# Kernel optimization log

Hardware: AMD Instinct MI355X
Metric: run time of the kernel (lower is better)

Reference implementation:

```python
import jax, jax.numpy as jnp
import numpy as np

B, L, ENC_IN, C_OUT = 8, 2048, 21, 21
D_MODEL, EXPAND, D_STATE, D_CONV = 512, 2, 16, 4
D_INNER = D_MODEL * EXPAND
DT_RANK = (D_MODEL + 15) // 16  # 'auto' => ceil(d_model/16) = 32
MARK_DIM = 4  # timeF features for freq='h'
PRED_LEN = 96


def setup_inputs() -> dict:
    key = jax.random.key(0)
    ks = jax.random.split(key, 13)
    s = 0.02
    return {
        'x_enc': jax.random.normal(ks[0], (B, L, ENC_IN), jnp.float32),
        'x_mark_enc': jax.random.normal(ks[1], (B, L, MARK_DIM), jnp.float32),
        'x_dec': jax.random.normal(ks[2], (B, PRED_LEN, ENC_IN), jnp.float32),
        'x_mark_dec': jax.random.normal(ks[3], (B, PRED_LEN, MARK_DIM), jnp.float32),
        'conv_w': jax.random.normal(ks[4], (D_MODEL, ENC_IN, 3), jnp.float32) * s,      # TokenEmbedding circular conv
        'temp_w': jax.random.normal(ks[5], (D_MODEL, MARK_DIM), jnp.float32) * s,       # TimeFeatureEmbedding (no bias)
        'in_proj_w': jax.random.normal(ks[6], (2 * D_INNER, D_MODEL), jnp.float32) * s,
        'conv1d_w': jax.random.normal(ks[7], (D_INNER, 1, D_CONV), jnp.float32) * s,    # depthwise causal conv
        'conv1d_b': jnp.zeros((D_INNER,), jnp.float32),
        'x_proj_w': jax.random.normal(ks[8], (DT_RANK + 2 * D_STATE, D_INNER), jnp.float32) * s,
        'dt_proj_w': jax.random.normal(ks[9], (D_INNER, DT_RANK), jnp.float32) * s,
        'dt_proj_b': jax.random.normal(ks[10], (D_INNER,), jnp.float32) * 0.1,
        'A_log': jnp.log(jnp.tile(jnp.arange(1, D_STATE + 1, dtype=jnp.float32), (D_INNER, 1))),  # mamba S4D-real init
        'D': jnp.ones((D_INNER,), jnp.float32),
        'out_proj_w': jax.random.normal(ks[11], (D_MODEL, D_INNER), jnp.float32) * s,
        'head_w': jax.random.normal(ks[12], (C_OUT, D_MODEL), jnp.float32) * s,
    }


def _pos_embedding(seq_len, d):
    pos = jnp.arange(seq_len, dtype=jnp.float32)[:, None]
    div = jnp.exp(jnp.arange(0, d, 2, dtype=jnp.float32) * (-np.log(10000.0) / d))
    pe = jnp.zeros((seq_len, d), jnp.float32)
    pe = pe.at[:, 0::2].set(jnp.sin(pos * div))
    pe = pe.at[:, 1::2].set(jnp.cos(pos * div))
    return pe


def _mamba(x, in_proj_w, conv1d_w, conv1d_b, x_proj_w, dt_proj_w, dt_proj_b, A_log, D):
    Bsz = x.shape[0]
    xz = x @ in_proj_w.T                          # (B,L,2*Din)
    xs, z = jnp.split(xz, 2, axis=-1)
    # causal depthwise conv1d over time (pad left d_conv-1, truncate to L)
    xc = jnp.pad(xs.transpose(0, 2, 1), ((0, 0), (0, 0), (D_CONV - 1, 0)))
    xc = jax.lax.conv_general_dilated(xc, conv1d_w, (1,), 'VALID',
                                      dimension_numbers=('NCH', 'OIH', 'NCH'),
                                      feature_group_count=D_INNER)
    xs = jax.nn.silu((xc + conv1d_b[None, :, None]).transpose(0, 2, 1))  # (B,L,Din)
    x_dbl = xs @ x_proj_w.T                       # (B,L,dt_rank+2N)
    dt, Bm, Cm = jnp.split(x_dbl, [DT_RANK, DT_RANK + D_STATE], axis=-1)
    delta = jax.nn.softplus(dt @ dt_proj_w.T + dt_proj_b)  # (B,L,Din)
    A = -jnp.exp(A_log)                           # (Din,N)

    def step(h, inp):
        u_t, d_t, b_t, c_t = inp                  # (B,Din),(B,Din),(B,N),(B,N)
        dA = jnp.exp(d_t[:, :, None] * A)         # (B,Din,N)
        h = dA * h + (d_t * u_t)[:, :, None] * b_t[:, None, :]
        return h, jnp.einsum('bdn,bn->bd', h, c_t)

    h0 = jnp.zeros((Bsz, D_INNER, D_STATE), xs.dtype)
    seq = (xs.transpose(1, 0, 2), delta.transpose(1, 0, 2),
           Bm.transpose(1, 0, 2), Cm.transpose(1, 0, 2))
    _, ys = jax.lax.scan(step, h0, seq)
    y = ys.transpose(1, 0, 2) + xs * D            # (B,L,Din)
    return y * jax.nn.silu(z)


def _forward(x_enc, x_mark_enc, conv_w, temp_w, in_proj_w, conv1d_w, conv1d_b,
             x_proj_w, dt_proj_w, dt_proj_b, A_log, D, out_proj_w, head_w):
    # RevIN-style instance norm over time (stats detached)
    mean = jax.lax.stop_gradient(jnp.mean(x_enc, axis=1, keepdims=True))
    xc = x_enc - mean
    std = jax.lax.stop_gradient(jnp.sqrt(jnp.var(xc, axis=1, keepdims=True) + 1e-5))
    xn = xc / std
    # TokenEmbedding: circular-padded conv1d, kernel 3, no bias
    xt = jnp.pad(xn.transpose(0, 2, 1), ((0, 0), (0, 0), (1, 1)), mode='wrap')
    val = jax.lax.conv_general_dilated(xt, conv_w, (1,), 'VALID',
                                       dimension_numbers=('NCH', 'OIH', 'NCH')).transpose(0, 2, 1)
    emb = val + x_mark_enc @ temp_w.T + _pos_embedding(x_enc.shape[1], D_MODEL)[None]
    y = _mamba(emb, in_proj_w, conv1d_w, conv1d_b, x_proj_w, dt_proj_w, dt_proj_b, A_log, D)
    y = y @ out_proj_w.T                          # Mamba out_proj (no bias)
    out = y @ head_w.T                            # final Linear (no bias)
    out = out * std + mean                        # de-normalize
    return out[:, -PRED_LEN:, :]


def reference(x_enc, x_mark_enc, x_dec, x_mark_dec, conv_w, temp_w, in_proj_w,
              conv1d_w, conv1d_b, x_proj_w, dt_proj_w, dt_proj_b, A_log, D,
              out_proj_w, head_w):
    # x_dec / x_mark_dec are accepted but unused by the forecast path
    return _forward(x_enc, x_mark_enc, conv_w, temp_w, in_proj_w, conv1d_w,
                    conv1d_b, x_proj_w, dt_proj_w, dt_proj_b, A_log, D,
                    out_proj_w, head_w)
```

## Files before the change

kernel.cpp:

```cpp
#include <hip/hip_runtime.h>
#include <hip/hip_bf16.h>
#include <math.h>

#define Bsz 8
#define Lseq 2048
#define ENC_IN 21
#define C_OUT 21
#define D_MODEL 512
#define D_INNER 1024
#define D_STATE 16
#define D_CONV 4
#define DT_RANK 32
#define MARK_DIM 4
#define PRED_LEN 96
#define L_TAIL (Lseq - PRED_LEN)
#define K_EMB 80
#define CHUNK 128
#define NCHUNK_A 15
#define MTOT (Bsz * Lseq)

#define PE_C0 (-9.210340371976184f / (float)D_MODEL)

typedef __attribute__((ext_vector_type(8))) short short8;
typedef __attribute__((ext_vector_type(4))) float f32x4;

__global__ void stats_kernel(const float* __restrict__ x_enc,
                             float* __restrict__ mean, float* __restrict__ stdv) {
    int bc = blockIdx.x;
    int b = bc / ENC_IN, c = bc % ENC_IN;
    __shared__ float red[256];
    int t = threadIdx.x;
    float s = 0.f;
    for (int l = t; l < Lseq; l += 256)
        s += x_enc[((size_t)b * Lseq + l) * ENC_IN + c];
    red[t] = s; __syncthreads();
    for (int off = 128; off > 0; off >>= 1) {
        if (t < off) red[t] += red[t + off];
        __syncthreads();
    }
    float m = red[0] / (float)Lseq;
    __syncthreads();
    float v = 0.f;
    for (int l = t; l < Lseq; l += 256) {
        float d = x_enc[((size_t)b * Lseq + l) * ENC_IN + c] - m;
        v += d * d;
    }
    red[t] = v; __syncthreads();
    for (int off = 128; off > 0; off >>= 1) {
        if (t < off) red[t] += red[t + off];
        __syncthreads();
    }
    if (t == 0) {
        mean[bc] = m;
        stdv[bc] = sqrtf(red[0] / (float)Lseq + 1e-5f);
    }
}

__global__ void fuse_w_kernel(const float* __restrict__ head_w,
                              const float* __restrict__ out_proj_w,
                              float* __restrict__ W) {
    int idx = blockIdx.x * 256 + threadIdx.x;
    if (idx >= C_OUT * D_INNER) return;
    int c = idx / D_INNER, d = idx % D_INNER;
    float s = 0.f;
    for (int k = 0; k < D_MODEL; ++k)
        s += head_w[c * D_MODEL + k] * out_proj_w[(size_t)k * D_INNER + d];
    W[idx] = s;
}

__global__ void prep_wT_kernel(const float* __restrict__ conv_w,
                               const float* __restrict__ temp_w,
                               float* __restrict__ WembT) {
    int idx = blockIdx.x * 256 + threadIdx.x;
    int k = idx / D_MODEL, d = idx % D_MODEL;
    float v = 0.f;
    if (k < 3 * ENC_IN) {
        int kk = k / ENC_IN, c = k % ENC_IN;
        v = conv_w[((size_t)d * ENC_IN + c) * 3 + kk];
    } else if (k < 3 * ENC_IN + MARK_DIM) {
        v = temp_w[d * MARK_DIM + (k - 3 * ENC_IN)];
    }
    WembT[idx] = v;
}

__global__ void prep_x_kernel(const float* __restrict__ x_enc,
                              const float* __restrict__ x_mark,
                              const float* __restrict__ mean,
                              const float* __restrict__ stdv,
                              float* __restrict__ xinT) {
    int idx = blockIdx.x * 256 + threadIdx.x;
    int k = idx >> 14, bl = idx & (MTOT - 1);
    int b = bl >> 11, l = bl & (Lseq - 1);
    float v = 0.f;
    if (k < 3 * ENC_IN) {
        int kk = k / ENC_IN, c = k % ENC_IN;
        int ll = (l + kk - 1 + Lseq) & (Lseq - 1);
        v = (x_enc[((size_t)b * Lseq + ll) * ENC_IN + c] - mean[b * ENC_IN + c])
            / stdv[b * ENC_IN + c];
    } else if (k < 3 * ENC_IN + MARK_DIM) {
        v = x_mark[((size_t)b * Lseq + l) * MARK_DIM + (k - 3 * ENC_IN)];
    }
    xinT[idx] = v;
}

__global__ void wcomb_kernel(const float* __restrict__ in_proj_w,
                             const float* __restrict__ WembT,
                             float* __restrict__ Wcomb) {
    int idx = blockIdx.x * 256 + threadIdx.x;
    int j = idx / K_EMB, k = idx % K_EMB;
    const float* a = in_proj_w + (size_t)j * D_MODEL;
    const float* b = WembT + (size_t)k * D_MODEL;
    float s = 0.f;
    for (int d = 0; d < D_MODEL; d += 4) {
        float4 av = *(const float4*)(a + d);
        float4 bv = *(const float4*)(b + d);
        s += av.x * bv.x + av.y * bv.y + av.z * bv.z + av.w * bv.w;
    }
    Wcomb[idx] = s;
}

__global__ void pepz_kernel(const float* __restrict__ in_proj_w,
                            float* __restrict__ PEpZ) {
    __shared__ float per[D_MODEL];
    int lz = blockIdx.x;
    int t = threadIdx.x;
    {
        int l = L_TAIL + lz;
        float div = __expf((float)(2 * t) * PE_C0);
        float s, c;
        sincosf((float)l * div, &s, &c);
        per[2 * t] = s;
        per[2 * t + 1] = c;
    }
    __syncthreads();
    for (int q = 0; q < 4; ++q) {
        int j = q * 256 + t;
        const float* w = in_proj_w + (size_t)(D_INNER + j) * D_MODEL;
        float s = 0.f;
        for (int d = 0; d < D_MODEL; d += 4) {
            float4 wv = *(const float4*)(w + d);
            s += per[d] * wv.x + per[d + 1] * wv.y + per[d + 2] * wv.z + per[d + 3] * wv.w;
        }
        PEpZ[(size_t)lz * D_INNER + j] = s;
    }
}

template <int AMODE, int BMODE, int EPI>
__launch_bounds__(256)
__global__ void gemm(const float* __restrict__ A, const float* __restrict__ B,
                     float* __restrict__ C0, const float* __restrict__ bias,
                     int M, int N, int K, int lda, int ldb) {
    __shared__ float As[16][65];
    __shared__ float Bs[16][65];
    int bm = blockIdx.y, bn = blockIdx.x;
    int t = threadIdx.x;
    int tx = t & 15, ty = t >> 4;
    float acc[4][4] = {};
    int arow = bm * 64, bcol = bn * 64;
    int lr = t >> 2;
    int lk = (t & 3) * 4;
    int lrk = t >> 4;
    int lm4 = (t & 15) * 4;

    size_t acol = 0;
    if constexpr (AMODE == 2) {
        int m0 = arow + lm4;
        acol = (size_t)(m0 / PRED_LEN) * Lseq + L_TAIL + (m0 % PRED_LEN);
    } else if constexpr (AMODE == 1) {
        acol = (size_t)(arow + lm4);
    }

    for (int k0 = 0; k0 < K; k0 += 16) {
        if constexpr (AMODE == 0) {
            float4 av = *(const float4*)(A + (size_t)(arow + lr) * lda + k0 + lk);
            As[lk + 0][lr] = av.x; As[lk + 1][lr] = av.y;
            As[lk + 2][lr] = av.z; As[lk + 3][lr] = av.w;
        } else {
            float4 av = *(const float4*)(A + (size_t)(k0 + lrk) * lda + acol);
            As[lrk][lm4 + 0] = av.x; As[lrk][lm4 + 1] = av.y;
            As[lrk][lm4 + 2] = av.z; As[lrk][lm4 + 3] = av.w;
        }
        if constexpr (BMODE == 0) {
            float4 bv = *(const float4*)(B + (size_t)(bcol + lr) * ldb + k0 + lk);
            Bs[lk + 0][lr] = bv.x; Bs[lk + 1][lr] = bv.y;
            Bs[lk + 2][lr] = bv.z; Bs[lk + 3][lr] = bv.w;
        } else {
            float4 bv = *(const float4*)(B + (size_t)(k0 + lrk) * ldb + bcol + lm4);
            Bs[lrk][lm4 + 0] = bv.x; Bs[lrk][lm4 + 1] = bv.y;
            Bs[lrk][lm4 + 2] = bv.z; Bs[lrk][lm4 + 3] = bv.w;
        }
        __syncthreads();
        #pragma unroll
        for (int kk = 0; kk < 16; ++kk) {
            float a[4], bq[4];
            #pragma unroll
            for (int i = 0; i < 4; ++i) a[i] = As[kk][ty * 4 + i];
            #pragma unroll
            for (int j = 0; j < 4; ++j) bq[j] = Bs[kk][tx * 4 + j];
            #pragma unroll
            for (int i = 0; i < 4; ++i)
                #pragma unroll
                for (int j = 0; j < 4; ++j)
                    acc[i][j] += a[i] * bq[j];
        }
        __syncthreads();
    }

    #pragma unroll
    for (int i = 0; i < 4; ++i) {
        int row = arow + ty * 4 + i;
        #pragma unroll
        for (int j = 0; j < 4; ++j) {
            int col = bcol + tx * 4 + j;
            float v = acc[i][j];
            if (EPI == 3) {
                v += bias[(size_t)(row % PRED_LEN) * N + col];
            }
            C0[(size_t)row * N + col] = v;
        }
    }
}

__device__ __forceinline__ void split_bf16(float x, short& hb, short& lb) {
    unsigned u = __float_as_uint(x);
    unsigned short h = (unsigned short)(u >> 16);
    float hf = __uint_as_float(((unsigned)h) << 16);
    unsigned short l = (unsigned short)(__float_as_uint(x - hf) >> 16);
    hb = (short)h; lb = (short)l;
}

template <int BMODE, int EPI>
__launch_bounds__(256)
__global__ void mfma_gemm(const float* __restrict__ A, const float* __restrict__ B,
                          float* __restrict__ C, const float* __restrict__ bias,
                          int M, int N, int K, int lda, int ldb) {
    __shared__ short Ah[64][48], Al[64][48];
    __shared__ short Bh[64][48], Bl[64][48];
    int t = threadIdx.x;
    int bn0 = blockIdx.x * 64;
    int am0 = blockIdx.y * 64;
    int w = t >> 6;
    int l = t & 63;
    int lr = l & 15;
    int lk = l >> 4;

    f32x4 acc[4];
    #pragma unroll
    for (int i = 0; i < 4; ++i) acc[i] = (f32x4){0.f, 0.f, 0.f, 0.f};

    const int mst = t >> 2, kst = (t & 3) * 8;

    for (int kb = 0; kb < K; kb += 32) {
        if (kb) __syncthreads();
        {
            const float* src = A + (size_t)(am0 + mst) * lda + kb + kst;
            short8 hv, lv;
            if (kb + 32 <= K) {
                float4 a0 = *(const float4*)(src);
                float4 a1 = *(const float4*)(src + 4);
                float xs[8] = {a0.x, a0.y, a0.z, a0.w, a1.x, a1.y, a1.z, a1.w};
                #pragma unroll
                for (int j = 0; j < 8; ++j) {
                    short hb, lb; split_bf16(xs[j], hb, lb);
                    hv[j] = hb; lv[j] = lb;
                }
            } else {
                #pragma unroll
                for (int j = 0; j < 8; ++j) {
                    float x = (kb + kst + j < K) ? src[j] : 0.f;
                    short hb, lb; split_bf16(x, hb, lb);
                    hv[j] = hb; lv[j] = lb;
                }
            }
            *(short8*)&Ah[mst][kst] = hv;
            *(short8*)&Al[mst][kst] = lv;
        }
        if constexpr (BMODE == 0) {
            short8 hv, lv;
            #pragma unroll
            for (int j = 0; j < 8; ++j) {
                int k = kb + kst + j;
                float x = (k < K) ? B[(size_t)k * ldb + bn0 + mst] : 0.f;
                short hb, lb; split_bf16(x, hb, lb);
                hv[j] = hb; lv[j] = lb;
            }
            *(short8*)&Bh[mst][kst] = hv;
            *(short8*)&Bl[mst][kst] = lv;
        } else {
            float ng = (float)(bn0 + mst);
            short8 hv, lv;
            #pragma unroll
            for (int p = 0; p < 4; ++p) {
                float e = __expf((float)(kb + kst + 2 * p) * PE_C0);
                float sv, cv;
                sincosf(ng * e, &sv, &cv);
                short hb, lb;
                split_bf16(sv, hb, lb); hv[2 * p] = hb; lv[2 * p] = lb;
                split_bf16(cv, hb, lb); hv[2 * p + 1] = hb; lv[2 * p + 1] = lb;
            }
            *(short8*)&Bh[mst][kst] = hv;
            *(short8*)&Bl[mst][kst] = lv;
        }
        __syncthreads();
        short8 a_hi = *(const short8*)&Ah[w * 16 + lr][lk * 8];
        short8 a_lo = *(const short8*)&Al[w * 16 + lr][lk * 8];
        #pragma unroll
        for (int t4 = 0; t4 < 4; ++t4) {
            short8 b_hi = *(const short8*)&Bh[t4 * 16 + lr][lk * 8];
            short8 b_lo = *(const short8*)&Bl[t4 * 16 + lr][lk * 8];
            acc[t4] = __builtin_amdgcn_mfma_f32_16x16x32_bf16(a_hi, b_hi, acc[t4], 0, 0, 0);
            acc[t4] = __builtin_amdgcn_mfma_f32_16x16x32_bf16(a_lo, b_hi, acc[t4], 0, 0, 0);
            acc[t4] = __builtin_amdgcn_mfma_f32_16x16x32_bf16(a_hi, b_lo, acc[t4], 0, 0, 0);
        }
    }

    #pragma unroll
    for (int t4 = 0; t4 < 4; ++t4) {
        #pragma unroll
        for (int r = 0; r < 4; ++r) {
            int row = am0 + w * 16 + lk * 4 + r;
            int col = bn0 + t4 * 16 + lr;
            float v = acc[t4][r];
            if (EPI == 1) {
                v += bias[row];
                v = (v > 20.f) ? v : log1pf(__expf(v));
            }
            if (EPI == 2) {
                v += bias[(size_t)row * Lseq + (col & (Lseq - 1))];
            }
            C[(size_t)row * N + col] = v;
        }
    }
}

__global__ void dwconv_kernel(const float* __restrict__ xs_rawT,
                              const float* __restrict__ w,
                              const float* __restrict__ bias,
                              float* __restrict__ outT) {
    int bid = blockIdx.x;
    int d = bid & (D_INNER - 1), ch = bid >> 10;
    int t = threadIdx.x;
    int lbase = ch * 1024 + t * 4;
    const float* row = xs_rawT + (size_t)d * MTOT;
    float w0 = w[d * D_CONV + 0], w1 = w[d * D_CONV + 1];
    float w2 = w[d * D_CONV + 2], w3 = w[d * D_CONV + 3];
    float bs = bias[d];
    float4 cur = *(const float4*)(row + lbase);
    float4 pv = make_float4(0.f, 0.f, 0.f, 0.f);
    if (lbase >= 4) pv = *(const float4*)(row + lbase - 4);
    float v[7] = {pv.y, pv.z, pv.w, cur.x, cur.y, cur.z, cur.w};
    int lpos = lbase & (Lseq - 1);
    float o[4];
    if (lpos != 0) {
        #pragma unroll
        for (int j = 0; j < 4; ++j)
            o[j] = bs + w0 * v[j] + w1 * v[j + 1] + w2 * v[j + 2] + w3 * v[j + 3];
    } else {
        #pragma unroll
        for (int j = 0; j < 4; ++j) {
            float acc = bs;
            #pragma unroll
            for (int k2 = 0; k2 < 4; ++k2) {
                int ll = j - 3 + k2;
                if (ll >= 0) acc += v[j + k2] * ((k2 == 0) ? w0 : (k2 == 1) ? w1 : (k2 == 2) ? w2 : w3);
            }
            o[j] = acc;
        }
    }
    float4 res;
    res.x = o[0] / (1.f + __expf(-o[0]));
    res.y = o[1] / (1.f + __expf(-o[1]));
    res.z = o[2] / (1.f + __expf(-o[2]));
    res.w = o[3] / (1.f + __expf(-o[3]));
    *(float4*)(outT + (size_t)d * MTOT + lbase) = res;
}

__launch_bounds__(256, 4)
__global__ void scanA_kernel(const float* __restrict__ deltaT,
                             const float* __restrict__ uT,
                             const float* __restrict__ xdblT,
                             const float* __restrict__ A_log,
                             float* __restrict__ Pa,
                             float* __restrict__ Sa) {
    int b = blockIdx.x >> 4;
    int dg = blockIdx.x & 15;
    int c = blockIdx.y;
    int t = threadIdx.x;
    int dgrp = t >> 4, n = t & 15;
    int d0 = dg * 64 + dgrp;

    float A[4], P[4], S[4];
    const float *pd[4], *pu[4];
    #pragma unroll
    for (int vd = 0; vd < 4; ++vd) {
        int d = d0 + 16 * vd;
        A[vd] = -__expf(A_log[d * D_STATE + n]);
        P[vd] = 1.f; S[vd] = 0.f;
        size_t base = (size_t)d * MTOT + b * Lseq + c * CHUNK;
        pd[vd] = deltaT + base;
        pu[vd] = uT + base;
    }
    const float* pB = xdblT + (size_t)(DT_RANK + n) * MTOT + b * Lseq + c * CHUNK;

    const int NI = CHUNK / 4;
    float4 BvA, dvA[4], uvA[4];
    float4 BvB, dvB[4], uvB[4];

    BvA = *(const float4*)(pB);
    #pragma unroll
    for (int vd = 0; vd < 4; ++vd) {
        dvA[vd] = *(const float4*)(pd[vd]);
        uvA[vd] = *(const float4*)(pu[vd]);
    }

    for (int i = 0; i < NI; i += 2) {
        BvB = *(const float4*)(pB + 4 * (i + 1));
        #pragma unroll
        for (int vd = 0; vd < 4; ++vd) {
            dvB[vd] = *(const float4*)(pd[vd] + 4 * (i + 1));
            uvB[vd] = *(const float4*)(pu[vd] + 4 * (i + 1));
        }
        #pragma unroll
        for (int vd = 0; vd < 4; ++vd) {
            float a;
            a = __expf(dvA[vd].x * A[vd]); P[vd] *= a; S[vd] = a * S[vd] + (dvA[vd].x * uvA[vd].x) * BvA.x;
            a = __expf(dvA[vd].y * A[vd]); P[vd] *= a; S[vd] = a * S[vd] + (dvA[vd].y * uvA[vd].y) * BvA.y;
            a = __expf(dvA[vd].z * A[vd]); P[vd] *= a; S[vd] = a * S[vd] + (dvA[vd].z * uvA[vd].z) * BvA.z;
            a = __expf(dvA[vd].w * A[vd]); P[vd] *= a; S[vd] = a * S[vd] + (dvA[vd].w * uvA[vd].w) * BvA.w;
        }
        int i2 = (i + 2 < NI) ? (i + 2) : (NI - 1);
        BvA = *(const float4*)(pB + 4 * i2);
        #pragma unroll
        for (int vd = 0; vd < 4; ++vd) {
            dvA[vd] = *(const float4*)(pd[vd] + 4 * i2);
            uvA[vd] = *(const float4*)(pu[vd] + 4 * i2);
        }
        #pragma unroll
        for (int vd = 0; vd < 4; ++vd) {
            float a;
            a = __expf(dvB[vd].x * A[vd]); P[vd] *= a; S[vd] = a * S[vd] + (dvB[vd].x * uvB[vd].x) * BvB.x;
            a = __expf(dvB[vd].y * A[vd]); P[vd] *= a; S[vd] = a * S[vd] + (dvB[vd].y * uvB[vd].y) * BvB.y;
            a = __expf(dvB[vd].z * A[vd]); P[vd] *= a; S[vd] = a * S[vd] + (dvB[vd].z * uvB[vd].z) * BvB.z;
            a = __expf(dvB[vd].w * A[vd]); P[vd] *= a; S[vd] = a * S[vd] + (dvB[vd].w * uvB[vd].w) * BvB.w;
        }
    }
    #pragma unroll
    for (int vd = 0; vd < 4; ++vd) {
        int d = d0 + 16 * vd;
        size_t o = ((size_t)(b * NCHUNK_A + c) * D_INNER + d) * 16 + n;
        Pa[o] = P[vd];
        Sa[o] = S[vd];
    }
}

__launch_bounds__(256)
__global__ void scanB_kernel(const float* __restrict__ deltaT,
                             const float* __restrict__ uT,
                             const float* __restrict__ xdblT,
                             const float* __restrict__ A_log,
                             const float* __restrict__ Dp,
                             const float* __restrict__ Pa,
                             const float* __restrict__ Sa,
                             const float* __restrict__ z96,
                             float* __restrict__ y96) {
    int b = blockIdx.x >> 6;
    int dg = blockIdx.x & 63;
    int t = threadIdx.x;
    int d = dg * 16 + (t >> 4);
    int n = t & 15;
    float A = -__expf(A_log[d * D_STATE + n]);
    float Dd = Dp[d];
    float h = 0.f;
    for (int c = 0; c < NCHUNK_A; ++c) {
        size_t o = ((size_t)(b * NCHUNK_A + c) * D_INNER + d) * 16 + n;
        h = Pa[o] * h + Sa[o];
    }
    const int lt0 = NCHUNK_A * CHUNK;
    size_t base = (size_t)d * MTOT + b * Lseq + lt0;
    const float* pd = deltaT + base;
    const float* pu = uT + base;
    const float* pB = xdblT + (size_t)(DT_RANK + n) * MTOT + b * Lseq + lt0;
    const float* pC = xdblT + (size_t)(DT_RANK + D_STATE + n) * MTOT + b * Lseq + lt0;

    #pragma unroll 2
    for (int i = 0; i < 8; ++i) {
        float4 dv = *(const float4*)(pd + 4 * i);
        float4 uv = *(const float4*)(pu + 4 * i);
        float4 Bv = *(const float4*)(pB + 4 * i);
        float a;
        a = __expf(dv.x * A); h = a * h + (dv.x * uv.x) * Bv.x;
        a = __expf(dv.y * A); h = a * h + (dv.y * uv.y) * Bv.y;
        a = __expf(dv.z * A); h = a * h + (dv.z * uv.z) * Bv.z;
        a = __expf(dv.w * A); h = a * h + (dv.w * uv.w) * Bv.w;
    }
    for (int i = 8; i < 32; ++i) {
        float4 dv = *(const float4*)(pd + 4 * i);
        float4 uv = *(const float4*)(pu + 4 * i);
        float4 Bv = *(const float4*)(pB + 4 * i);
        float4 Cv = *(const float4*)(pC + 4 * i);
        #pragma unroll
        for (int j = 0; j < 4; ++j) {
            float dl = (j == 0) ? dv.x : (j == 1) ? dv.y : (j == 2) ? dv.z : dv.w;
            float uu = (j == 0) ? uv.x : (j == 1) ? uv.y : (j == 2) ? uv.z : uv.w;
            float Bb = (j == 0) ? Bv.x : (j == 1) ? Bv.y : (j == 2) ? Bv.z : Bv.w;
            float Cc = (j == 0) ? Cv.x : (j == 1) ? Cv.y : (j == 2) ? Cv.z : Cv.w;
            float a = __expf(dl * A);
            h = a * h + (dl * uu) * Bb;
            float y = h * Cc;
            #pragma unroll
            for (int m = 8; m >= 1; m >>= 1) y += __shfl_xor(y, m, 16);
            if (n == 0) {
                int lz = (lt0 + 4 * i + j) - L_TAIL;
                size_t o = ((size_t)b * PRED_LEN + lz) * D_INNER + d;
                float z = z96[o];
                y96[o] = (y + uu * Dd) * (z / (1.f + __expf(-z)));
            }
        }
    }
}

__global__ void head_kernel(const float* __restrict__ y96,
                            const float* __restrict__ W,
                            const float* __restrict__ mean,
                            const float* __restrict__ stdv,
                            float* __restrict__ out) {
    int idx = blockIdx.x;
    int c = idx % C_OUT;
    int bt = idx / C_OUT;
    int b = bt / PRED_LEN;
    int lane = threadIdx.x;
    const float* yrow = y96 + (size_t)bt * D_INNER;
    const float* wrow = W + (size_t)c * D_INNER;
    float s = 0.f;
    for (int d = lane; d < D_INNER; d += 64) s += yrow[d] * wrow[d];
    #pragma unroll
    for (int m = 32; m >= 1; m >>= 1) s += __shfl_xor(s, m, 64);
    if (lane == 0)
        out[(size_t)bt * C_OUT + c] = s * stdv[b * C_OUT + c] + mean[b * C_OUT + c];
}

extern "C" void kernel_launch(void* const* d_in, const int* in_sizes, int n_in,
                              void* d_out, int out_size, void* d_ws, size_t ws_size,
                              hipStream_t stream) {
    const float* x_enc     = (const float*)d_in[0];
    const float* x_mark    = (const float*)d_in[1];
    const float* conv_w    = (const float*)d_in[4];
    const float* temp_w    = (const float*)d_in[5];
    const float* in_proj_w = (const float*)d_in[6];
    const float* conv1d_w  = (const float*)d_in[7];
    const float* conv1d_b  = (const float*)d_in[8];
    const float* x_proj_w  = (const float*)d_in[9];
    const float* dt_proj_w = (const float*)d_in[10];
    const float* dt_proj_b = (const float*)d_in[11];
    const float* A_log     = (const float*)d_in[12];
    const float* Dp        = (const float*)d_in[13];
    const float* out_proj_w= (const float*)d_in[14];
    const float* head_w    = (const float*)d_in[15];
    float* out = (float*)d_out;
    float* ws = (float*)d_ws;

    size_t off = 0;
    float* mean     = ws + off; off += 256;
    float* stdv     = ws + off; off += 256;
    float* W        = ws + off; off += (size_t)C_OUT * D_INNER;
    float* WembT    = ws + off; off += (size_t)K_EMB * D_MODEL;
    float* Wcomb    = ws + off; off += (size_t)2 * D_INNER * K_EMB;
    float* PEpT     = ws + off; off += (size_t)D_INNER * Lseq;
    float* PEpZ     = ws + off; off += (size_t)PRED_LEN * D_INNER;
    float* xinT     = ws + off; off += (size_t)K_EMB * MTOT;
    float* xs_rawT  = ws + off; off += (size_t)D_INNER * MTOT;
    float* z96      = ws + off; off += (size_t)Bsz * PRED_LEN * D_INNER;
    float* xs_convT = ws + off; off += (size_t)D_INNER * MTOT;
    float* xdblT    = ws + off; off += (size_t)64 * MTOT;
    float* deltaT   = ws + off; off += (size_t)D_INNER * MTOT;
    float* Pa       = ws + off; off += (size_t)Bsz * NCHUNK_A * D_INNER * D_STATE;
    float* Sa       = ws + off; off += (size_t)Bsz * NCHUNK_A * D_INNER * D_STATE;
    float* y96      = ws + off; off += (size_t)Bsz * PRED_LEN * D_INNER;

    stats_kernel<<<Bsz * ENC_IN, 256, 0, stream>>>(x_enc, mean, stdv);
    fuse_w_kernel<<<(C_OUT * D_INNER + 255) / 256, 256, 0, stream>>>(head_w, out_proj_w, W);
    prep_wT_kernel<<<(K_EMB * D_MODEL) / 256, 256, 0, stream>>>(conv_w, temp_w, WembT);
    prep_x_kernel<<<(K_EMB * MTOT) / 256, 256, 0, stream>>>(x_enc, x_mark, mean, stdv, xinT);
    wcomb_kernel<<<(2 * D_INNER * K_EMB) / 256, 256, 0, stream>>>(in_proj_w, WembT, Wcomb);
    pepz_kernel<<<PRED_LEN, 256, 0, stream>>>(in_proj_w, PEpZ);
    mfma_gemm<1, 0><<<dim3(Lseq / 64, D_INNER / 64), 256, 0, stream>>>(
        in_proj_w, nullptr, PEpT, nullptr, D_INNER, Lseq, D_MODEL, D_MODEL, 0);
    mfma_gemm<0, 2><<<dim3(MTOT / 64, D_INNER / 64), 256, 0, stream>>>(
        Wcomb, xinT, xs_rawT, PEpT, D_INNER, MTOT, K_EMB, K_EMB, MTOT);
    gemm<2, 0, 3><<<dim3(D_INNER / 64, (Bsz * PRED_LEN) / 64), 256, 0, stream>>>(
        xinT, Wcomb + (size_t)D_INNER * K_EMB, z96, PEpZ,
        Bsz * PRED_LEN, D_INNER, K_EMB, MTOT, K_EMB);
    dwconv_kernel<<<D_INNER * 16, 256, 0, stream>>>(xs_rawT, conv1d_w, conv1d_b, xs_convT);
    mfma_gemm<0, 0><<<dim3(MTOT / 64, 1), 256, 0, stream>>>(
        x_proj_w, xs_convT, xdblT, nullptr, 64, MTOT, D_INNER, D_INNER, MTOT);
    mfma_gemm<0, 1><<<dim3(MTOT / 64, D_INNER / 64), 256, 0, stream>>>(
        dt_proj_w, xdblT, deltaT, dt_proj_b, D_INNER, MTOT, DT_RANK, DT_RANK, MTOT);
    scanA_kernel<<<dim3(Bsz * 16, NCHUNK_A), 256, 0, stream>>>(
        deltaT, xs_convT, xdblT, A_log, Pa, Sa);
    scanB_kernel<<<Bsz * 64, 256, 0, stream>>>(
        deltaT, xs_convT, xdblT, A_log, Dp, Pa, Sa, z96, y96);
    head_kernel<<<Bsz * PRED_LEN * C_OUT, 64, 0, stream>>>(y96, W, mean, stdv, out);
}
```

Before: 504.3 us.

## Use 128-row MFMA GEMM tiles and split-K atomics for x_proj GEMM

Replaces the 64x64 split-bf16 MFMA GEMM with a 128x64 tile variant, so each B tile loaded and converted into shared memory is reused across twice as many rows of A. This cuts B global loads and bf16 split conversions for the in_proj, positional-embedding and dt_proj GEMMs. The x_proj GEMM (M=64, K=1024) previously launched only 256 blocks. It now splits K four ways with atomicAdd into a pre-zeroed output to raise parallelism. The cost is an extra zeroing kernel, atomic traffic, nondeterministic summation order, and higher register and LDS use per block.

```diff
diff --git a/kernel.cpp b/kernel.cpp
--- a/kernel.cpp
+++ b/kernel.cpp
@@ -231,29 +231,31 @@
 
 template <int BMODE, int EPI>
 __launch_bounds__(256)
-__global__ void mfma_gemm(const float* __restrict__ A, const float* __restrict__ B,
-                          float* __restrict__ C, const float* __restrict__ bias,
-                          int M, int N, int K, int lda, int ldb) {
-    __shared__ short Ah[64][48], Al[64][48];
+__global__ void mfma_gemm128(const float* __restrict__ A, const float* __restrict__ B,
+                             float* __restrict__ C, const float* __restrict__ bias,
+                             int M, int N, int K, int lda, int ldb) {
+    __shared__ short Ah[128][48], Al[128][48];
     __shared__ short Bh[64][48], Bl[64][48];
     int t = threadIdx.x;
     int bn0 = blockIdx.x * 64;
-    int am0 = blockIdx.y * 64;
-    int w = t >> 6;
-    int l = t & 63;
-    int lr = l & 15;
-    int lk = l >> 4;
-
-    f32x4 acc[4];
-    #pragma unroll
-    for (int i = 0; i < 4; ++i) acc[i] = (f32x4){0.f, 0.f, 0.f, 0.f};
+    int am0 = blockIdx.y * 128;
+    int w = t >> 6, l = t & 63;
+    int lr = l & 15, lk = l >> 4;
+
+    f32x4 acc[2][4];
+    #pragma unroll
+    for (int i = 0; i < 2; ++i)
+        #pragma unroll
+        for (int j = 0; j < 4; ++j) acc[i][j] = (f32x4){0.f, 0.f, 0.f, 0.f};
 
     const int mst = t >> 2, kst = (t & 3) * 8;
 
     for (int kb = 0; kb < K; kb += 32) {
         if (kb) __syncthreads();
-        {
-            const float* src = A + (size_t)(am0 + mst) * lda + kb + kst;
+        #pragma unroll
+        for (int half = 0; half < 2; ++half) {
+            int m = mst + half * 64;
+            const float* src = A + (size_t)(am0 + m) * lda + kb + kst;
             short8 hv, lv;
             if (kb + 32 <= K) {
                 float4 a0 = *(const float4*)(src);
@@ -272,8 +274,8 @@
                     hv[j] = hb; lv[j] = lb;
                 }
             }
-            *(short8*)&Ah[mst][kst] = hv;
-            *(short8*)&Al[mst][kst] = lv;
+            *(short8*)&Ah[m][kst] = hv;
+            *(short8*)&Al[m][kst] = lv;
         }
         if constexpr (BMODE == 0) {
             short8 hv, lv;
@@ -302,6 +304,91 @@
             *(short8*)&Bl[mst][kst] = lv;
         }
         __syncthreads();
+        #pragma unroll
+        for (int mt = 0; mt < 2; ++mt) {
+            short8 a_hi = *(const short8*)&Ah[mt * 64 + w * 16 + lr][lk * 8];
+            short8 a_lo = *(const short8*)&Al[mt * 64 + w * 16 + lr][lk * 8];
+            #pragma unroll
+            for (int t4 = 0; t4 < 4; ++t4) {
+                short8 b_hi = *(const short8*)&Bh[t4 * 16 + lr][lk * 8];
+                short8 b_lo = *(const short8*)&Bl[t4 * 16 + lr][lk * 8];
+                acc[mt][t4] = __builtin_amdgcn_mfma_f32_16x16x32_bf16(a_hi, b_hi, acc[mt][t4], 0, 0, 0);
+                acc[mt][t4] = __builtin_amdgcn_mfma_f32_16x16x32_bf16(a_lo, b_hi, acc[mt][t4], 0, 0, 0);
+                acc[mt][t4] = __builtin_amdgcn_mfma_f32_16x16x32_bf16(a_hi, b_lo, acc[mt][t4], 0, 0, 0);
+            }
+        }
+    }
+
+    #pragma unroll
+    for (int mt = 0; mt < 2; ++mt) {
+        #pragma unroll
+        for (int t4 = 0; t4 < 4; ++t4) {
+            #pragma unroll
+            for (int r = 0; r < 4; ++r) {
+                int row = am0 + mt * 64 + w * 16 + lk * 4 + r;
+                int col = bn0 + t4 * 16 + lr;
+                float v = acc[mt][t4][r];
+                if (EPI == 1) {
+                    v += bias[row];
+                    v = (v > 20.f) ? v : log1pf(__expf(v));
+                }
+                if (EPI == 2) {
+                    v += bias[(size_t)row * Lseq + (col & (Lseq - 1))];
+                }
+                C[(size_t)row * N + col] = v;
+            }
+        }
+    }
+}
+
+__launch_bounds__(256)
+__global__ void mfma_gemm_splitk(const float* __restrict__ A, const float* __restrict__ B,
+                                 float* __restrict__ C,
+                                 int M, int N, int K, int lda, int ldb, int ksplit) {
+    __shared__ short Ah[64][48], Al[64][48];
+    __shared__ short Bh[64][48], Bl[64][48];
+    int t = threadIdx.x;
+    int bn0 = blockIdx.x * 64;
+    int kz0 = blockIdx.z * ksplit;
+    int kz1 = min(K, kz0 + ksplit);
+    int w = t >> 6, l = t & 63;
+    int lr = l & 15, lk = l >> 4;
+
+    f32x4 acc[4];
+    #pragma unroll
+    for (int i = 0; i < 4; ++i) acc[i] = (f32x4){0.f, 0.f, 0.f, 0.f};
+
+    const int mst = t >> 2, kst = (t & 3) * 8;
+
+    for (int kb = kz0; kb < kz1; kb += 32) {
+        if (kb != kz0) __syncthreads();
+        {
+            const float* src = A + (size_t)mst * lda + kb + kst;
+            float4 a0 = *(const float4*)(src);
+            float4 a1 = *(const float4*)(src + 4);
+            float xs[8] = {a0.x, a0.y, a0.z, a0.w, a1.x, a1.y, a1.z, a1.w};
+            short8 hv, lv;
+            #pragma unroll
+            for (int j = 0; j < 8; ++j) {
+                short hb, lb; split_bf16(xs[j], hb, lb);
+                hv[j] = hb; lv[j] = lb;
+            }
+            *(short8*)&Ah[mst][kst] = hv;
+            *(short8*)&Al[mst][kst] = lv;
+        }
+        {
+            short8 hv, lv;
+            #pragma unroll
+            for (int j = 0; j < 8; ++j) {
+                int k = kb + kst + j;
+                float x = B[(size_t)k * ldb + bn0 + mst];
+                short hb, lb; split_bf16(x, hb, lb);
+                hv[j] = hb; lv[j] = lb;
+            }
+            *(short8*)&Bh[mst][kst] = hv;
+            *(short8*)&Bl[mst][kst] = lv;
+        }
+        __syncthreads();
         short8 a_hi = *(const short8*)&Ah[w * 16 + lr][lk * 8];
         short8 a_lo = *(const short8*)&Al[w * 16 + lr][lk * 8];
         #pragma unroll
@@ -318,19 +405,15 @@
     for (int t4 = 0; t4 < 4; ++t4) {
         #pragma unroll
         for (int r = 0; r < 4; ++r) {
-            int row = am0 + w * 16 + lk * 4 + r;
+            int row = w * 16 + lk * 4 + r;
             int col = bn0 + t4 * 16 + lr;
-            float v = acc[t4][r];
-            if (EPI == 1) {
-                v += bias[row];
-                v = (v > 20.f) ? v : log1pf(__expf(v));
-            }
-            if (EPI == 2) {
-                v += bias[(size_t)row * Lseq + (col & (Lseq - 1))];
-            }
-            C[(size_t)row * N + col] = v;
-        }
-    }
+            atomicAdd(&C[(size_t)row * N + col], acc[t4][r]);
+        }
+    }
+}
+
+__global__ void zero_kernel(float4* __restrict__ p) {
+    p[(size_t)blockIdx.x * 256 + threadIdx.x] = make_float4(0.f, 0.f, 0.f, 0.f);
 }
 
 __global__ void dwconv_kernel(const float* __restrict__ xs_rawT,
@@ -583,17 +666,18 @@
     prep_x_kernel<<<(K_EMB * MTOT) / 256, 256, 0, stream>>>(x_enc, x_mark, mean, stdv, xinT);
     wcomb_kernel<<<(2 * D_INNER * K_EMB) / 256, 256, 0, stream>>>(in_proj_w, WembT, Wcomb);
     pepz_kernel<<<PRED_LEN, 256, 0, stream>>>(in_proj_w, PEpZ);
-    mfma_gemm<1, 0><<<dim3(Lseq / 64, D_INNER / 64), 256, 0, stream>>>(
+    mfma_gemm128<1, 0><<<dim3(Lseq / 64, D_INNER / 128), 256, 0, stream>>>(
         in_proj_w, nullptr, PEpT, nullptr, D_INNER, Lseq, D_MODEL, D_MODEL, 0);
-    mfma_gemm<0, 2><<<dim3(MTOT / 64, D_INNER / 64), 256, 0, stream>>>(
+    mfma_gemm128<0, 2><<<dim3(MTOT / 64, D_INNER / 128), 256, 0, stream>>>(
         Wcomb, xinT, xs_rawT, PEpT, D_INNER, MTOT, K_EMB, K_EMB, MTOT);
     gemm<2, 0, 3><<<dim3(D_INNER / 64, (Bsz * PRED_LEN) / 64), 256, 0, stream>>>(
         xinT, Wcomb + (size_t)D_INNER * K_EMB, z96, PEpZ,
         Bsz * PRED_LEN, D_INNER, K_EMB, MTOT, K_EMB);
     dwconv_kernel<<<D_INNER * 16, 256, 0, stream>>>(xs_rawT, conv1d_w, conv1d_b, xs_convT);
-    mfma_gemm<0, 0><<<dim3(MTOT / 64, 1), 256, 0, stream>>>(
-        x_proj_w, xs_convT, xdblT, nullptr, 64, MTOT, D_INNER, D_INNER, MTOT);
-    mfma_gemm<0, 1><<<dim3(MTOT / 64, D_INNER / 64), 256, 0, stream>>>(
+    zero_kernel<<<(64 * MTOT) / 4 / 256, 256, 0, stream>>>((float4*)xdblT);
+    mfma_gemm_splitk<<<dim3(MTOT / 64, 1, 4), 256, 0, stream>>>(
+        x_proj_w, xs_convT, xdblT, 64, MTOT, D_INNER, D_INNER, MTOT, 256);
+    mfma_gemm128<0, 1><<<dim3(MTOT / 64, D_INNER / 128), 256, 0, stream>>>(
         dt_proj_w, xdblT, deltaT, dt_proj_b, D_INNER, MTOT, DT_RANK, DT_RANK, MTOT);
     scanA_kernel<<<dim3(Bsz * 16, NCHUNK_A), 256, 0, stream>>>(
         deltaT, xs_convT, xdblT, A_log, Pa, Sa);
```

New measurement: 504.5 us. About the same (+0.0%).
